# Optimization experiments

Measured on AMD Instinct MI355X. Metric: run time of the kernel, lower is better.

## Reference

```python
import jax, jax.numpy as jnp
import numpy as np

N = 50000      # nodes
E2 = 400000    # undirected edges
E = 2 * E2     # directed edges (each undirected edge in both directions)
DIN = 512      # input feature dim
DH = 128       # MLP hidden
C = 8          # num classes / BP channels


def setup_inputs() -> dict:
    key = jax.random.key(0)
    ks = jax.random.split(key, 9)
    x = jax.random.normal(ks[0], (N, DIN), jnp.float32)
    src0 = jax.random.randint(ks[1], (E2,), 0, N)
    dst0 = jax.random.randint(ks[2], (E2,), 0, N)
    # symmetric directed edge list: row 0 = source j, row 1 = target i
    edge_index = jnp.stack([jnp.concatenate([src0, dst0]),
                            jnp.concatenate([dst0, src0])])
    w0 = jax.random.uniform(ks[3], (E2,), jnp.float32, 0.5, 1.5)
    edge_weight = jnp.concatenate([w0, w0])  # reverse edge shares weight
    # edge_rv[e] = index of the reverse of edge e
    edge_rv = jnp.concatenate([jnp.arange(E2) + E2, jnp.arange(E2)])
    W1 = jax.random.normal(ks[4], (DIN, DH), jnp.float32) * 0.05
    b1 = jnp.zeros((DH,), jnp.float32)
    W2 = jax.random.normal(ks[5], (DH, C), jnp.float32) * 0.05
    b2 = jnp.zeros((C,), jnp.float32)
    param = jax.random.normal(ks[6], (C, C), jnp.float32) * 0.1
    return {"x": x, "edge_index": edge_index, "edge_weight": edge_weight,
            "edge_rv": edge_rv, "W1": W1, "b1": b1, "W2": W2, "b2": b2,
            "param": param, "K": 5}


def log_normalize(log_x):
    return log_x - jax.nn.logsumexp(log_x, axis=-1, keepdims=True)


def reference(x, edge_index, edge_weight, edge_rv, W1, b1, W2, b2, param, K):
    # MLP transform + LogSoftmax -> initial log-beliefs [N, C]
    h = jax.nn.relu(x @ W1 + b1)
    log_b0 = jax.nn.log_softmax(h @ W2 + b2, axis=-1)

    # learn_H=True: logH = logsigmoid(param + param^T), [C, C]
    logH = jax.nn.log_sigmoid(param + param.T)
    src, dst = edge_index[0], edge_index[1]
    # per-edge coupling matrix [E, C, C]
    logC = edge_weight[:, None, None] * logH[None, :, :]

    log_b = log_b0
    log_msg = None
    for _ in range(K):
        x_j = log_b[src]                       # gather source beliefs [E, C]
        if log_msg is not None:
            x_j = x_j - log_msg[edge_rv]       # remove reverse message
        # tropical-semiring matvec in log domain: logsumexp over source channel
        log_msg = log_normalize(jax.nn.logsumexp(x_j[:, :, None] + logC, axis=1))
        agg = jax.ops.segment_sum(log_msg, dst, num_segments=N)  # scatter-add
        log_b = log_normalize(log_b0 + agg)
    return log_b
```

## Files before the change

kernel.cpp:

```cpp
#include <hip/hip_runtime.h>
#include <hip/hip_bf16.h>
#include <hip/hip_fp16.h>
#include <math.h>

#define NN 50000
#define EE 800000
#define E2K 400000
#define DINK 512
#define DHK 128
#define CK 8
#define KIT 5
#define NBLKS 196
#define NPB 32
#define CAP 1024

typedef __attribute__((ext_vector_type(8))) short short8;
typedef __attribute__((ext_vector_type(4))) float f32x4;

__device__ __forceinline__ unsigned short f2bf(float f) {
    union { float f; unsigned int u; } v;
    v.f = f;
    unsigned int u = v.u;
    unsigned int r = (u + 0x7FFFu + ((u >> 16) & 1u)) >> 16;
    return (unsigned short)r;
}
__device__ __forceinline__ float bfu2f(unsigned int lo16) {
    union { unsigned int u; float f; } v;
    v.u = lo16 << 16;
    return v.f;
}

__global__ __launch_bounds__(256) void prep_kernel(
    const float* __restrict__ W1, const float* __restrict__ param,
    unsigned short* __restrict__ W1t, float* __restrict__ logH) {
    if (blockIdx.x < 256) {
        int idx = blockIdx.x * 256 + threadIdx.x;
        int n = idx >> 9;
        int k = idx & 511;
        W1t[idx] = f2bf(W1[(size_t)k * DHK + n]);
    } else if (threadIdx.x < 64) {
        int t = threadIdx.x;
        int i = t >> 3, j = t & 7;
        float z = param[i * 8 + j] + param[j * 8 + i];
        logH[t] = fminf(z, 0.0f) - log1pf(expf(-fabsf(z)));
    }
}

__global__ __launch_bounds__(256) void mlp_mfma_kernel(
    const float* __restrict__ x, const unsigned short* __restrict__ W1t,
    const float* __restrict__ b1, const float* __restrict__ W2,
    const float* __restrict__ b2, float* __restrict__ logb0) {
    __shared__ unsigned short hs[128 * 136];
    __shared__ float W2s[128 * 8];
    __shared__ float b1s[128];
    __shared__ float b2s[8];

    const int tid = threadIdx.x;
    const int wave = tid >> 6;
    const int lane = tid & 63;
    const int q = lane >> 4;
    const int lm = lane & 15;
    const int wm = wave >> 1, wn = wave & 1;
    const int n0 = blockIdx.x * 128;

    if (tid < 128) b1s[tid] = b1[tid];
    if (tid < 8) b2s[tid] = b2[tid];
    {
        int i = tid * 4;
        *(float4*)&W2s[i] = *(const float4*)&W2[i];
    }
    __syncthreads();

    const float* xptr[4];
#pragma unroll
    for (int mt = 0; mt < 4; ++mt) {
        int r = n0 + wm * 64 + mt * 16 + lm;
        if (r > NN - 1) r = NN - 1;
        xptr[mt] = x + (size_t)r * DINK + q * 8;
    }
    const unsigned short* bptr[4];
#pragma unroll
    for (int nt = 0; nt < 4; ++nt) {
        int c = wn * 64 + nt * 16 + lm;
        bptr[nt] = W1t + (size_t)c * DINK + q * 8;
    }

    f32x4 acc[4][4];
#pragma unroll
    for (int mt = 0; mt < 4; ++mt)
#pragma unroll
        for (int nt = 0; nt < 4; ++nt) acc[mt][nt] = (f32x4){0.f, 0.f, 0.f, 0.f};

    float4 ar[4][2];
    short8 bc[4];
#pragma unroll
    for (int mt = 0; mt < 4; ++mt) {
        ar[mt][0] = *(const float4*)(xptr[mt]);
        ar[mt][1] = *(const float4*)(xptr[mt] + 4);
    }
#pragma unroll
    for (int nt = 0; nt < 4; ++nt) bc[nt] = *(const short8*)(bptr[nt]);

#pragma unroll
    for (int k0 = 32; k0 <= DINK; k0 += 32) {
        float4 ar2[4][2];
        short8 b2f[4];
        if (k0 < DINK) {
#pragma unroll
            for (int mt = 0; mt < 4; ++mt) {
                ar2[mt][0] = *(const float4*)(xptr[mt] + k0);
                ar2[mt][1] = *(const float4*)(xptr[mt] + k0 + 4);
            }
#pragma unroll
            for (int nt = 0; nt < 4; ++nt)
                b2f[nt] = *(const short8*)(bptr[nt] + k0);
        }
        short8 af[4];
#pragma unroll
        for (int mt = 0; mt < 4; ++mt) {
            union { short8 s; __hip_bfloat162 h[4]; } cv;
            cv.h[0] = __float22bfloat162_rn(make_float2(ar[mt][0].x, ar[mt][0].y));
            cv.h[1] = __float22bfloat162_rn(make_float2(ar[mt][0].z, ar[mt][0].w));
            cv.h[2] = __float22bfloat162_rn(make_float2(ar[mt][1].x, ar[mt][1].y));
            cv.h[3] = __float22bfloat162_rn(make_float2(ar[mt][1].z, ar[mt][1].w));
            af[mt] = cv.s;
        }
#pragma unroll
        for (int mt = 0; mt < 4; ++mt)
#pragma unroll
            for (int nt = 0; nt < 4; ++nt)
                acc[mt][nt] = __builtin_amdgcn_mfma_f32_16x16x32_bf16(
                    af[mt], bc[nt], acc[mt][nt], 0, 0, 0);
        if (k0 < DINK) {
#pragma unroll
            for (int mt = 0; mt < 4; ++mt) {
                ar[mt][0] = ar2[mt][0];
                ar[mt][1] = ar2[mt][1];
            }
#pragma unroll
            for (int nt = 0; nt < 4; ++nt) bc[nt] = b2f[nt];
        }
    }

#pragma unroll
    for (int nt = 0; nt < 4; ++nt) {
        int j = wn * 64 + nt * 16 + lm;
        float bj = b1s[j];
#pragma unroll
        for (int mt = 0; mt < 4; ++mt) {
            int rbase = wm * 64 + mt * 16 + q * 4;
#pragma unroll
            for (int r = 0; r < 4; ++r) {
                float h = fmaxf(acc[mt][nt][r] + bj, 0.0f);
                hs[(rbase + r) * 136 + j] = f2bf(h);
            }
        }
    }
    __syncthreads();

    int row = tid >> 1;
    int half = tid & 1;
    const unsigned short* hp = &hs[row * 136 + half * 64];
    float p[8] = {0.f, 0.f, 0.f, 0.f, 0.f, 0.f, 0.f, 0.f};
#pragma unroll
    for (int ch = 0; ch < 8; ++ch) {
        uint4 c4 = *(const uint4*)(hp + ch * 8);
        unsigned int uu[4] = {c4.x, c4.y, c4.z, c4.w};
#pragma unroll
        for (int p2 = 0; p2 < 4; ++p2) {
            float h0 = bfu2f(uu[p2] & 0xFFFFu);
            float h1 = bfu2f(uu[p2] >> 16);
            int j = half * 64 + ch * 8 + p2 * 2;
            const float* w0 = &W2s[j * 8];
            const float* w1 = &W2s[(j + 1) * 8];
#pragma unroll
            for (int c = 0; c < 8; ++c) p[c] = fmaf(h0, w0[c], p[c]);
#pragma unroll
            for (int c = 0; c < 8; ++c) p[c] = fmaf(h1, w1[c], p[c]);
        }
    }
#pragma unroll
    for (int c = 0; c < 8; ++c) p[c] += __shfl_xor(p[c], 1, 64);
    int grow = n0 + row;
    if (half == 0 && grow < NN) {
        float v[8];
        float mx = -1e30f;
#pragma unroll
        for (int c = 0; c < 8; ++c) {
            v[c] = p[c] + b2s[c];
            mx = fmaxf(mx, v[c]);
        }
        float s = 0.0f;
#pragma unroll
        for (int c = 0; c < 8; ++c) s += expf(v[c] - mx);
        float ln = mx + logf(s);
        float4* p0 = (float4*)&logb0[(size_t)grow * 8];
        p0[0] = make_float4(v[0] - ln, v[1] - ln, v[2] - ln, v[3] - ln);
        p0[1] = make_float4(v[4] - ln, v[5] - ln, v[6] - ln, v[7] - ln);
    }
}


__global__ __launch_bounds__(256) void deg_pair_kernel(const int* __restrict__ ei,
                                                       int* __restrict__ cnt) {
    int e = blockIdx.x * 256 + threadIdx.x;
    if (e >= E2K) return;
    int s = ei[e];
    int d = ei[EE + e];
    atomicAdd(&cnt[d], 1);
    atomicAdd(&cnt[s], 1);
}

__global__ __launch_bounds__(256) void scan_partial_kernel(
    const int* __restrict__ cnt, int* __restrict__ partial) {
    __shared__ int sd[256];
    int t = threadIdx.x;
    int i = blockIdx.x * 256 + t;
    sd[t] = (i < NN) ? cnt[i] : 0;
    __syncthreads();
#pragma unroll
    for (int s = 128; s > 0; s >>= 1) {
        if (t < s) sd[t] += sd[t + s];
        __syncthreads();
    }
    if (t == 0) partial[blockIdx.x] = sd[0];
}

__global__ __launch_bounds__(256) void scan_tops_kernel(
    const int* __restrict__ partial, int* __restrict__ tops) {
    __shared__ int sd[256];
    int t = threadIdx.x;
    sd[t] = (t < NBLKS) ? partial[t] : 0;
    __syncthreads();
#pragma unroll
    for (int s = 1; s < 256; s <<= 1) {
        int a = sd[t];
        int b = (t >= s) ? sd[t - s] : 0;
        __syncthreads();
        sd[t] = a + b;
        __syncthreads();
    }
    if (t < NBLKS) tops[t] = (t > 0) ? sd[t - 1] : 0;
}

__global__ __launch_bounds__(256) void scan_write_kernel(
    const int* __restrict__ cnt, const int* __restrict__ tops,
    int* __restrict__ off) {
    __shared__ int sd[256];
    int t = threadIdx.x;
    int i = blockIdx.x * 256 + t;
    int v = (i < NN) ? cnt[i] : 0;
    sd[t] = v;
    __syncthreads();
#pragma unroll
    for (int s = 1; s < 256; s <<= 1) {
        int a = sd[t];
        int b = (t >= s) ? sd[t - s] : 0;
        __syncthreads();
        sd[t] = a + b;
        __syncthreads();
    }
    if (i < NN) off[i] = tops[blockIdx.x] + sd[t] - v;
    if (i == NN - 1) off[NN] = EE;
}

__global__ __launch_bounds__(256) void pos_pair_kernel(
    const int* __restrict__ ei, const float* __restrict__ ew,
    const int* __restrict__ off, int* __restrict__ cnt,
    int2* __restrict__ perm_sw, int2* __restrict__ perm_dr) {
    int e = blockIdx.x * 256 + threadIdx.x;
    if (e >= E2K) return;
    int s = ei[e];
    int d = ei[EE + e];
    int wbits = __float_as_int(ew[e]);
    int pA = off[d] + atomicAdd(&cnt[d], 1);
    int pB = off[s] + atomicAdd(&cnt[s], 1);
    int2 v;
    v.x = s; v.y = wbits; perm_sw[pA] = v;
    v.x = d;              perm_sw[pB] = v;
    v.x = d; v.y = pB;    perm_dr[pA] = v;
    v.x = s; v.y = pA;    perm_dr[pB] = v;
}

__global__ __launch_bounds__(256) void bp_iter_kernel(
    const float* __restrict__ logb0, const int* __restrict__ off,
    const int2* __restrict__ perm_sw, const int2* __restrict__ perm_dr,
    const float* __restrict__ logH, const uint4* __restrict__ xin_cur,
    uint4* __restrict__ xin_next, float* __restrict__ out,
    int first, int last) {
    __shared__ _Float16 smg[CAP * 8];
    __shared__ float sb[NPB * 8];
    __shared__ float lH[64];
    const int t = threadIdx.x;
    if (t < 64) lH[t] = logH[t];

    const int n0 = blockIdx.x * NPB;
    const int nend = (n0 + NPB < NN) ? (n0 + NPB) : NN;
    const int jb0 = off[n0];
    const int jb1 = off[nend];
    const int nl = t >> 3;
    const int c = t & 7;
    const int n = n0 + nl;

    float a = 0.0f;
    int jn0 = 0, jn1 = 0;
    if (n < nend) {
        jn0 = off[n];
        jn1 = off[n + 1];
        a = logb0[(size_t)n * 8 + c];
    }
    __syncthreads();

    const int single = (jb1 - jb0) <= CAP;

    for (int cb = jb0; cb < jb1; cb += CAP) {
        int ce = (cb + CAP < jb1) ? (cb + CAP) : jb1;
        for (int j = cb + t; j < ce; j += 256) {
            int2 sw = perm_sw[j];
            float w = __int_as_float(sw.y);
            float xj[8];
            if (first) {
                const float4* pb = (const float4*)&logb0[(size_t)sw.x * 8];
                float4 v0 = pb[0], v1 = pb[1];
                xj[0] = v0.x; xj[1] = v0.y; xj[2] = v0.z; xj[3] = v0.w;
                xj[4] = v1.x; xj[5] = v1.y; xj[6] = v1.z; xj[7] = v1.w;
            } else {
                union { uint4 u; _Float16 h[8]; } cv;
                cv.u = xin_cur[j];
#pragma unroll
                for (int k = 0; k < 8; ++k) xj[k] = (float)cv.h[k];
            }
            float M = xj[0];
#pragma unroll
            for (int k = 1; k < 8; ++k) M = fmaxf(M, xj[k]);
#pragma unroll
            for (int k = 0; k < 8; ++k) xj[k] -= M;
            float mg[8];
#pragma unroll
            for (int c2 = 0; c2 < 8; ++c2) {
                float ssum = 0.0f;
#pragma unroll
                for (int c1 = 0; c1 < 8; ++c1)
                    ssum += __expf(fmaf(w, lH[c1 * 8 + c2], xj[c1]));
                mg[c2] = __logf(ssum);
            }
            float mm = mg[0];
#pragma unroll
            for (int k = 1; k < 8; ++k) mm = fmaxf(mm, mg[k]);
            float se = 0.0f;
#pragma unroll
            for (int k = 0; k < 8; ++k) se += __expf(mg[k] - mm);
            float ln = mm + __logf(se);
            union { uint4 u; _Float16 h[8]; } ov;
#pragma unroll
            for (int k = 0; k < 8; ++k) ov.h[k] = (_Float16)(mg[k] - ln);
            *(uint4*)&smg[(j - cb) * 8] = ov.u;
        }
        __syncthreads();
        int lo = (jn0 > cb) ? jn0 : cb;
        int hi = (jn1 < ce) ? jn1 : ce;
        for (int j = lo; j < hi; ++j) a += (float)smg[(j - cb) * 8 + c];
        __syncthreads();
    }

    float mx = a;
#pragma unroll
    for (int s = 1; s < 8; s <<= 1) mx = fmaxf(mx, __shfl_xor(mx, s, 8));
    float sum = __expf(a - mx);
#pragma unroll
    for (int s = 1; s < 8; s <<= 1) sum += __shfl_xor(sum, s, 8);
    float v = a - (mx + __logf(sum));
    if (n < nend) {
        if (last) out[(size_t)n * 8 + c] = v;
        sb[nl * 8 + c] = v;
    }
    if (last) return;
    __syncthreads();

    for (int cb = jb0; cb < jb1; cb += CAP) {
        int ce = (cb + CAP < jb1) ? (cb + CAP) : jb1;
        if (!single) {
            for (int j = cb + t; j < ce; j += 256) {
                int2 sw = perm_sw[j];
                float w = __int_as_float(sw.y);
                float xj[8];
                if (first) {
                    const float4* pb = (const float4*)&logb0[(size_t)sw.x * 8];
                    float4 v0 = pb[0], v1 = pb[1];
                    xj[0] = v0.x; xj[1] = v0.y; xj[2] = v0.z; xj[3] = v0.w;
                    xj[4] = v1.x; xj[5] = v1.y; xj[6] = v1.z; xj[7] = v1.w;
                } else {
                    union { uint4 u; _Float16 h[8]; } cv;
                    cv.u = xin_cur[j];
#pragma unroll
                    for (int k = 0; k < 8; ++k) xj[k] = (float)cv.h[k];
                }
                float M = xj[0];
#pragma unroll
                for (int k = 1; k < 8; ++k) M = fmaxf(M, xj[k]);
#pragma unroll
                for (int k = 0; k < 8; ++k) xj[k] -= M;
                float mg[8];
#pragma unroll
                for (int c2 = 0; c2 < 8; ++c2) {
                    float ssum = 0.0f;
#pragma unroll
                    for (int c1 = 0; c1 < 8; ++c1)
                        ssum += __expf(fmaf(w, lH[c1 * 8 + c2], xj[c1]));
                    mg[c2] = __logf(ssum);
                }
                float mm = mg[0];
#pragma unroll
                for (int k = 1; k < 8; ++k) mm = fmaxf(mm, mg[k]);
                float se = 0.0f;
#pragma unroll
                for (int k = 0; k < 8; ++k) se += __expf(mg[k] - mm);
                float ln = mm + __logf(se);
                union { uint4 u; _Float16 h[8]; } ov;
#pragma unroll
                for (int k = 0; k < 8; ++k) ov.h[k] = (_Float16)(mg[k] - ln);
                *(uint4*)&smg[(j - cb) * 8] = ov.u;
            }
            __syncthreads();
        }
        _Float16* xinh = (_Float16*)xin_next;
        int items = (ce - cb) * 8;
        for (int item = t; item < items; item += 256) {
            int j = cb + (item >> 3);
            int c2 = item & 7;
            int2 dr = perm_dr[j];
            int dl = dr.x - n0;
            float val = sb[dl * 8 + c2] - (float)smg[(j - cb) * 8 + c2];
            xinh[(size_t)dr.y * 8 + c2] = (_Float16)val;
        }
        if (!single) __syncthreads();
    }
}

extern "C" void kernel_launch(void* const* d_in, const int* in_sizes, int n_in,
                              void* d_out, int out_size, void* d_ws, size_t ws_size,
                              hipStream_t stream) {
    const float* x = (const float*)d_in[0];
    const int* ei = (const int*)d_in[1];
    const float* ew = (const float*)d_in[2];
    const float* W1 = (const float*)d_in[4];
    const float* b1 = (const float*)d_in[5];
    const float* W2 = (const float*)d_in[6];
    const float* b2 = (const float*)d_in[7];
    const float* param = (const float*)d_in[8];
    float* out = (float*)d_out;

    float* wsf = (float*)d_ws;
    float* logH = wsf;
    float* logb0 = logH + 64;
    uint4* xinA = (uint4*)(logb0 + (size_t)NN * 8);
    uint4* xinB = xinA + EE;
    int* off = (int*)(xinB + EE);
    int2* perm_sw = (int2*)(off + (NN + 1));
    int2* perm_dr = perm_sw + EE;
    unsigned short* W1t = (unsigned short*)(perm_dr + EE);
    int* cnt = (int*)xinA;
    int* partial = cnt + NN;
    int* tops = partial + NBLKS;

    prep_kernel<<<257, 256, 0, stream>>>(W1, param, W1t, logH);
    mlp_mfma_kernel<<<(NN + 127) / 128, 256, 0, stream>>>(x, W1t, b1, W2, b2,
                                                          logb0);

    const int E2B = (E2K + 255) / 256;

    hipMemsetAsync(cnt, 0, (size_t)NN * sizeof(int), stream);
    deg_pair_kernel<<<E2B, 256, 0, stream>>>(ei, cnt);
    scan_partial_kernel<<<NBLKS, 256, 0, stream>>>(cnt, partial);
    scan_tops_kernel<<<1, 256, 0, stream>>>(partial, tops);
    scan_write_kernel<<<NBLKS, 256, 0, stream>>>(cnt, tops, off);
    hipMemsetAsync(cnt, 0, (size_t)NN * sizeof(int), stream);
    pos_pair_kernel<<<E2B, 256, 0, stream>>>(ei, ew, off, cnt, perm_sw, perm_dr);

    const int NB = (NN + NPB - 1) / NPB;
    uint4* cur = xinA;
    uint4* nxt = xinB;
    for (int it = 0; it < KIT; ++it) {
        bp_iter_kernel<<<NB, 256, 0, stream>>>(
            logb0, off, perm_sw, perm_dr, logH, cur, nxt, out,
            it == 0 ? 1 : 0, it == KIT - 1 ? 1 : 0);
        uint4* tmp = cur; cur = nxt; nxt = tmp;
    }
}
```

Before: 427.9 us.

## Store per-edge messages and node beliefs instead of precomputed cavity inputs

BP iterations now write normalized per-edge messages sequentially and per-node beliefs. The next iteration gathers the source belief and subtracts the reverse message, instead of precomputing cavity inputs with a scattered second pass. This removes the recompute pass for large chunks and the scattered fp16 writes, at the cost of random gathers of beliefs and reverse messages. The MLP kernel also uses 64-row tiles to double the block count.

```diff
diff --git a/kernel.cpp b/kernel.cpp
--- a/kernel.cpp
+++ b/kernel.cpp
@@ -50,7 +50,7 @@
     const float* __restrict__ x, const unsigned short* __restrict__ W1t,
     const float* __restrict__ b1, const float* __restrict__ W2,
     const float* __restrict__ b2, float* __restrict__ logb0) {
-    __shared__ unsigned short hs[128 * 136];
+    __shared__ unsigned short hs[64 * 136];
     __shared__ float W2s[128 * 8];
     __shared__ float b1s[128];
     __shared__ float b2s[8];
@@ -61,7 +61,7 @@
     const int q = lane >> 4;
     const int lm = lane & 15;
     const int wm = wave >> 1, wn = wave & 1;
-    const int n0 = blockIdx.x * 128;
+    const int n0 = blockIdx.x * 64;
 
     if (tid < 128) b1s[tid] = b1[tid];
     if (tid < 8) b2s[tid] = b2[tid];
@@ -71,10 +71,10 @@
     }
     __syncthreads();
 
-    const float* xptr[4];
-#pragma unroll
-    for (int mt = 0; mt < 4; ++mt) {
-        int r = n0 + wm * 64 + mt * 16 + lm;
+    const float* xptr[2];
+#pragma unroll
+    for (int mt = 0; mt < 2; ++mt) {
+        int r = n0 + wm * 32 + mt * 16 + lm;
         if (r > NN - 1) r = NN - 1;
         xptr[mt] = x + (size_t)r * DINK + q * 8;
     }
@@ -85,16 +85,16 @@
         bptr[nt] = W1t + (size_t)c * DINK + q * 8;
     }
 
-    f32x4 acc[4][4];
-#pragma unroll
-    for (int mt = 0; mt < 4; ++mt)
+    f32x4 acc[2][4];
+#pragma unroll
+    for (int mt = 0; mt < 2; ++mt)
 #pragma unroll
         for (int nt = 0; nt < 4; ++nt) acc[mt][nt] = (f32x4){0.f, 0.f, 0.f, 0.f};
 
-    float4 ar[4][2];
+    float4 ar[2][2];
     short8 bc[4];
 #pragma unroll
-    for (int mt = 0; mt < 4; ++mt) {
+    for (int mt = 0; mt < 2; ++mt) {
         ar[mt][0] = *(const float4*)(xptr[mt]);
         ar[mt][1] = *(const float4*)(xptr[mt] + 4);
     }
@@ -103,11 +103,11 @@
 
 #pragma unroll
     for (int k0 = 32; k0 <= DINK; k0 += 32) {
-        float4 ar2[4][2];
+        float4 ar2[2][2];
         short8 b2f[4];
         if (k0 < DINK) {
 #pragma unroll
-            for (int mt = 0; mt < 4; ++mt) {
+            for (int mt = 0; mt < 2; ++mt) {
                 ar2[mt][0] = *(const float4*)(xptr[mt] + k0);
                 ar2[mt][1] = *(const float4*)(xptr[mt] + k0 + 4);
             }
@@ -115,9 +115,9 @@
             for (int nt = 0; nt < 4; ++nt)
                 b2f[nt] = *(const short8*)(bptr[nt] + k0);
         }
-        short8 af[4];
-#pragma unroll
-        for (int mt = 0; mt < 4; ++mt) {
+        short8 af[2];
+#pragma unroll
+        for (int mt = 0; mt < 2; ++mt) {
             union { short8 s; __hip_bfloat162 h[4]; } cv;
             cv.h[0] = __float22bfloat162_rn(make_float2(ar[mt][0].x, ar[mt][0].y));
             cv.h[1] = __float22bfloat162_rn(make_float2(ar[mt][0].z, ar[mt][0].w));
@@ -126,14 +126,14 @@
             af[mt] = cv.s;
         }
 #pragma unroll
-        for (int mt = 0; mt < 4; ++mt)
+        for (int mt = 0; mt < 2; ++mt)
 #pragma unroll
             for (int nt = 0; nt < 4; ++nt)
                 acc[mt][nt] = __builtin_amdgcn_mfma_f32_16x16x32_bf16(
                     af[mt], bc[nt], acc[mt][nt], 0, 0, 0);
         if (k0 < DINK) {
 #pragma unroll
-            for (int mt = 0; mt < 4; ++mt) {
+            for (int mt = 0; mt < 2; ++mt) {
                 ar[mt][0] = ar2[mt][0];
                 ar[mt][1] = ar2[mt][1];
             }
@@ -147,8 +147,8 @@
         int j = wn * 64 + nt * 16 + lm;
         float bj = b1s[j];
 #pragma unroll
-        for (int mt = 0; mt < 4; ++mt) {
-            int rbase = wm * 64 + mt * 16 + q * 4;
+        for (int mt = 0; mt < 2; ++mt) {
+            int rbase = wm * 32 + mt * 16 + q * 4;
 #pragma unroll
             for (int r = 0; r < 4; ++r) {
                 float h = fmaxf(acc[mt][nt][r] + bj, 0.0f);
@@ -158,19 +158,19 @@
     }
     __syncthreads();
 
-    int row = tid >> 1;
-    int half = tid & 1;
-    const unsigned short* hp = &hs[row * 136 + half * 64];
+    int row = tid >> 2;
+    int qh = tid & 3;
+    const unsigned short* hp = &hs[row * 136 + qh * 32];
     float p[8] = {0.f, 0.f, 0.f, 0.f, 0.f, 0.f, 0.f, 0.f};
 #pragma unroll
-    for (int ch = 0; ch < 8; ++ch) {
+    for (int ch = 0; ch < 4; ++ch) {
         uint4 c4 = *(const uint4*)(hp + ch * 8);
         unsigned int uu[4] = {c4.x, c4.y, c4.z, c4.w};
 #pragma unroll
         for (int p2 = 0; p2 < 4; ++p2) {
             float h0 = bfu2f(uu[p2] & 0xFFFFu);
             float h1 = bfu2f(uu[p2] >> 16);
-            int j = half * 64 + ch * 8 + p2 * 2;
+            int j = qh * 32 + ch * 8 + p2 * 2;
             const float* w0 = &W2s[j * 8];
             const float* w1 = &W2s[(j + 1) * 8];
 #pragma unroll
@@ -181,8 +181,10 @@
     }
 #pragma unroll
     for (int c = 0; c < 8; ++c) p[c] += __shfl_xor(p[c], 1, 64);
+#pragma unroll
+    for (int c = 0; c < 8; ++c) p[c] += __shfl_xor(p[c], 2, 64);
     int grow = n0 + row;
-    if (half == 0 && grow < NN) {
+    if (qh == 0 && grow < NN) {
         float v[8];
         float mx = -1e30f;
 #pragma unroll
@@ -285,11 +287,11 @@
 __global__ __launch_bounds__(256) void bp_iter_kernel(
     const float* __restrict__ logb0, const int* __restrict__ off,
     const int2* __restrict__ perm_sw, const int2* __restrict__ perm_dr,
-    const float* __restrict__ logH, const uint4* __restrict__ xin_cur,
-    uint4* __restrict__ xin_next, float* __restrict__ out,
+    const float* __restrict__ logH, const uint4* __restrict__ msg_prev,
+    uint4* __restrict__ msg_next, const float* __restrict__ bel_prev,
+    float* __restrict__ bel_next, float* __restrict__ out,
     int first, int last) {
     __shared__ _Float16 smg[CAP * 8];
-    __shared__ float sb[NPB * 8];
     __shared__ float lH[64];
     const int t = threadIdx.x;
     if (t < 64) lH[t] = logH[t];
@@ -311,24 +313,22 @@
     }
     __syncthreads();
 
-    const int single = (jb1 - jb0) <= CAP;
-
     for (int cb = jb0; cb < jb1; cb += CAP) {
         int ce = (cb + CAP < jb1) ? (cb + CAP) : jb1;
         for (int j = cb + t; j < ce; j += 256) {
             int2 sw = perm_sw[j];
             float w = __int_as_float(sw.y);
+            const float4* pb = (const float4*)&bel_prev[(size_t)sw.x * 8];
+            float4 v0 = pb[0], v1 = pb[1];
             float xj[8];
-            if (first) {
-                const float4* pb = (const float4*)&logb0[(size_t)sw.x * 8];
-                float4 v0 = pb[0], v1 = pb[1];
-                xj[0] = v0.x; xj[1] = v0.y; xj[2] = v0.z; xj[3] = v0.w;
-                xj[4] = v1.x; xj[5] = v1.y; xj[6] = v1.z; xj[7] = v1.w;
-            } else {
-                union { uint4 u; _Float16 h[8]; } cv;
-                cv.u = xin_cur[j];
-#pragma unroll
-                for (int k = 0; k < 8; ++k) xj[k] = (float)cv.h[k];
+            xj[0] = v0.x; xj[1] = v0.y; xj[2] = v0.z; xj[3] = v0.w;
+            xj[4] = v1.x; xj[5] = v1.y; xj[6] = v1.z; xj[7] = v1.w;
+            if (!first) {
+                int rvp = perm_dr[j].y;
+                union { uint4 u; _Float16 h[8]; } mv;
+                mv.u = msg_prev[rvp];
+#pragma unroll
+                for (int k = 0; k < 8; ++k) xj[k] -= (float)mv.h[k];
             }
             float M = xj[0];
 #pragma unroll
@@ -355,6 +355,7 @@
 #pragma unroll
             for (int k = 0; k < 8; ++k) ov.h[k] = (_Float16)(mg[k] - ln);
             *(uint4*)&smg[(j - cb) * 8] = ov.u;
+            if (!last) msg_next[j] = ov.u;
         }
         __syncthreads();
         int lo = (jn0 > cb) ? jn0 : cb;
@@ -372,68 +373,7 @@
     float v = a - (mx + __logf(sum));
     if (n < nend) {
         if (last) out[(size_t)n * 8 + c] = v;
-        sb[nl * 8 + c] = v;
-    }
-    if (last) return;
-    __syncthreads();
-
-    for (int cb = jb0; cb < jb1; cb += CAP) {
-        int ce = (cb + CAP < jb1) ? (cb + CAP) : jb1;
-        if (!single) {
-            for (int j = cb + t; j < ce; j += 256) {
-                int2 sw = perm_sw[j];
-                float w = __int_as_float(sw.y);
-                float xj[8];
-                if (first) {
-                    const float4* pb = (const float4*)&logb0[(size_t)sw.x * 8];
-                    float4 v0 = pb[0], v1 = pb[1];
-                    xj[0] = v0.x; xj[1] = v0.y; xj[2] = v0.z; xj[3] = v0.w;
-                    xj[4] = v1.x; xj[5] = v1.y; xj[6] = v1.z; xj[7] = v1.w;
-                } else {
-                    union { uint4 u; _Float16 h[8]; } cv;
-                    cv.u = xin_cur[j];
-#pragma unroll
-                    for (int k = 0; k < 8; ++k) xj[k] = (float)cv.h[k];
-                }
-                float M = xj[0];
-#pragma unroll
-                for (int k = 1; k < 8; ++k) M = fmaxf(M, xj[k]);
-#pragma unroll
-                for (int k = 0; k < 8; ++k) xj[k] -= M;
-                float mg[8];
-#pragma unroll
-                for (int c2 = 0; c2 < 8; ++c2) {
-                    float ssum = 0.0f;
-#pragma unroll
-                    for (int c1 = 0; c1 < 8; ++c1)
-                        ssum += __expf(fmaf(w, lH[c1 * 8 + c2], xj[c1]));
-                    mg[c2] = __logf(ssum);
-                }
-                float mm = mg[0];
-#pragma unroll
-                for (int k = 1; k < 8; ++k) mm = fmaxf(mm, mg[k]);
-                float se = 0.0f;
-#pragma unroll
-                for (int k = 0; k < 8; ++k) se += __expf(mg[k] - mm);
-                float ln = mm + __logf(se);
-                union { uint4 u; _Float16 h[8]; } ov;
-#pragma unroll
-                for (int k = 0; k < 8; ++k) ov.h[k] = (_Float16)(mg[k] - ln);
-                *(uint4*)&smg[(j - cb) * 8] = ov.u;
-            }
-            __syncthreads();
-        }
-        _Float16* xinh = (_Float16*)xin_next;
-        int items = (ce - cb) * 8;
-        for (int item = t; item < items; item += 256) {
-            int j = cb + (item >> 3);
-            int c2 = item & 7;
-            int2 dr = perm_dr[j];
-            int dl = dr.x - n0;
-            float val = sb[dl * 8 + c2] - (float)smg[(j - cb) * 8 + c2];
-            xinh[(size_t)dr.y * 8 + c2] = (_Float16)val;
-        }
-        if (!single) __syncthreads();
+        else bel_next[(size_t)n * 8 + c] = v;
     }
 }
 
@@ -453,19 +393,21 @@
     float* wsf = (float*)d_ws;
     float* logH = wsf;
     float* logb0 = logH + 64;
-    uint4* xinA = (uint4*)(logb0 + (size_t)NN * 8);
-    uint4* xinB = xinA + EE;
-    int* off = (int*)(xinB + EE);
-    int2* perm_sw = (int2*)(off + (NN + 1));
+    uint4* msgA = (uint4*)(logb0 + (size_t)NN * 8);
+    uint4* msgB = msgA + EE;
+    int* off = (int*)(msgB + EE);
+    int2* perm_sw = (int2*)(off + 50004);
     int2* perm_dr = perm_sw + EE;
     unsigned short* W1t = (unsigned short*)(perm_dr + EE);
-    int* cnt = (int*)xinA;
+    float* belA = (float*)(W1t + 65536);
+    float* belB = belA + (size_t)NN * 8;
+    int* cnt = (int*)msgA;
     int* partial = cnt + NN;
     int* tops = partial + NBLKS;
 
     prep_kernel<<<257, 256, 0, stream>>>(W1, param, W1t, logH);
-    mlp_mfma_kernel<<<(NN + 127) / 128, 256, 0, stream>>>(x, W1t, b1, W2, b2,
-                                                          logb0);
+    mlp_mfma_kernel<<<(NN + 63) / 64, 256, 0, stream>>>(x, W1t, b1, W2, b2,
+                                                        logb0);
 
     const int E2B = (E2K + 255) / 256;
 
@@ -478,12 +420,15 @@
     pos_pair_kernel<<<E2B, 256, 0, stream>>>(ei, ew, off, cnt, perm_sw, perm_dr);
 
     const int NB = (NN + NPB - 1) / NPB;
-    uint4* cur = xinA;
-    uint4* nxt = xinB;
+    uint4* msgs[2] = {msgA, msgB};
+    float* bels[2] = {belA, belB};
+    const float* bprev = logb0;
     for (int it = 0; it < KIT; ++it) {
         bp_iter_kernel<<<NB, 256, 0, stream>>>(
-            logb0, off, perm_sw, perm_dr, logH, cur, nxt, out,
+            logb0, off, perm_sw, perm_dr, logH,
+            msgs[(it + 1) & 1] , msgs[it & 1] ,
+            bprev, bels[it & 1], out,
             it == 0 ? 1 : 0, it == KIT - 1 ? 1 : 0);
-        uint4* tmp = cur; cur = nxt; nxt = tmp;
-    }
-}
+        bprev = bels[it & 1];
+    }
+}
```

Result: slower. 466.6 us (+9.0%).
